# Optimization experiments

Measured on AMD Instinct MI355X. Metric: run time of the kernel, lower is better.

## Reference

```python
import jax, jax.numpy as jnp
import numpy as np

DIM = 1024
N_HEADS = 16
HEAD_DIM = DIM // N_HEADS


def setup_inputs() -> dict:
    key = jax.random.key(0)
    ks = jax.random.split(key, 6)
    s = DIM ** -0.5
    return {
        "x": jax.random.normal(ks[0], (2, 2048, DIM), dtype=jnp.float32),
        "Wq": jax.random.normal(ks[1], (DIM, DIM), dtype=jnp.float32) * s,
        "Wk": jax.random.normal(ks[2], (DIM, DIM), dtype=jnp.float32) * s,
        "Wv": jax.random.normal(ks[3], (DIM, DIM), dtype=jnp.float32) * s,
        "Wo": jax.random.normal(ks[4], (DIM, DIM), dtype=jnp.float32) * s,
        "bo": jax.random.normal(ks[5], (DIM,), dtype=jnp.float32) * 0.01,
    }


def reference(x, Wq, Wk, Wv, Wo, bo):
    B, T, C = x.shape
    H, D = N_HEADS, HEAD_DIM
    # Linear(dim, dim, bias=False): y = x @ W^T
    q = (x @ Wq.T).reshape(B, T, H, D).transpose(0, 2, 1, 3)  # B H T D
    k = (x @ Wk.T).reshape(B, T, H, D).transpose(0, 2, 1, 3)
    v = (x @ Wv.T).reshape(B, T, H, D).transpose(0, 2, 1, 3)
    q = q * (D ** -0.5)
    attn = jnp.einsum('bhqd,bhkd->bhqk', q, k)  # B H T T
    causal_mask = jnp.triu(jnp.ones((T, T), dtype=bool), k=1)
    attn = jnp.where(causal_mask, -jnp.inf, attn)
    attn = jax.nn.softmax(attn, axis=-1)
    out = jnp.einsum('bhqk,bhkd->bhqd', attn, v)  # B H T D
    out = out.transpose(0, 2, 1, 3).reshape(B, T, C)
    return out @ Wo.T + bo
```

## Files before the change

kernel.cpp:

```cpp
#include <hip/hip_runtime.h>
#include <math.h>

typedef __attribute__((ext_vector_type(8))) short bf16x8;
typedef __attribute__((ext_vector_type(4))) float f32x4;

__device__ __forceinline__ ushort f2bf(float f) {
  union { float f; unsigned u; } v; v.f = f;
  return (ushort)((v.u + 0x8000u) >> 16);
}

__device__ __forceinline__ void g2l16(const void* g, void* l) {
  __builtin_amdgcn_global_load_lds((const __attribute__((address_space(1))) unsigned*)g,
                                   (__attribute__((address_space(3))) unsigned*)l, 16, 0, 0);
}

__global__ __launch_bounds__(256) void cast_x_kernel(const float* __restrict__ x,
                                                     ushort* __restrict__ o, int n4) {
  int i = blockIdx.x * 256 + threadIdx.x;
  if (i >= n4) return;
  float4 v = ((const float4*)x)[i];
  ushort4 u; u.x = f2bf(v.x); u.y = f2bf(v.y); u.z = f2bf(v.z); u.w = f2bf(v.w);
  ((ushort4*)o)[i] = u;
}

__global__ __launch_bounds__(256) void cast_w_kernel(const float* __restrict__ Wq,
                                                     const float* __restrict__ Wk,
                                                     const float* __restrict__ Wv,
                                                     const float* __restrict__ Wo,
                                                     ushort* __restrict__ o) {
  int i = blockIdx.x * 256 + threadIdx.x;
  int row = i >> 8;
  int sel = row >> 10;
  const float* src = (sel == 0) ? Wq : (sel == 1) ? Wk : (sel == 2) ? Wv : Wo;
  float scale = (sel == 0) ? 0.125f * 1.44269504088896f : 1.0f;
  float4 v = ((const float4*)src)[i & 0x3FFFF];
  ushort4 u;
  u.x = f2bf(v.x * scale); u.y = f2bf(v.y * scale);
  u.z = f2bf(v.z * scale); u.w = f2bf(v.w * scale);
  ((ushort4*)o)[i] = u;
}

template<int BN, bool BF16_OUT, bool BIAS, bool SPLIT>
__global__ __launch_bounds__(256) void gemm_bt(const ushort* __restrict__ A,
                                               const ushort* __restrict__ B,
                                               void* __restrict__ Cout,
                                               const float* __restrict__ bias,
                                               int M, int N, int K) {
  __shared__ __align__(16) ushort As[2][128 * 32];
  __shared__ __align__(16) ushort Bs[2][BN * 32];
  const int m0 = blockIdx.y * 128, n0 = blockIdx.x * BN;
  const int tid = threadIdx.x, lane = tid & 63, wid = tid >> 6;
  const int quad = lane >> 4, lc = lane & 15;
  const int lrow = lane >> 2, lcol = (lane & 3) * 8;
  const int wm = (BN == 128) ? (wid >> 1) * 64 : wid * 32;
  const int wn = (BN == 128) ? (wid & 1) * 64 : 0;
  constexpr int MT = (BN == 128) ? 4 : 2;

  f32x4 acc[MT][4] = {};

  auto stage = [&](int k0, int nb) {
    const ushort* Ag = A + (size_t)(m0 + wid * 32 + lrow) * K + k0 + lcol;
    g2l16(Ag, &As[nb][wid * 1024]);
    g2l16(Ag + (size_t)16 * K, &As[nb][wid * 1024 + 512]);
    if constexpr (BN == 128) {
      const ushort* Bg = B + (size_t)(n0 + wid * 32 + lrow) * K + k0 + lcol;
      g2l16(Bg, &Bs[nb][wid * 1024]);
      g2l16(Bg + (size_t)16 * K, &Bs[nb][wid * 1024 + 512]);
    } else {
      const ushort* Bg = B + (size_t)(n0 + wid * 16 + lrow) * K + k0 + lcol;
      g2l16(Bg, &Bs[nb][wid * 512]);
    }
  };

  stage(0, 0);
  for (int k0 = 0; k0 < K; k0 += 32) {
    const int nb = (k0 >> 5) & 1;
    __syncthreads();
    if (k0 + 32 < K) stage(k0 + 32, nb ^ 1);

    bf16x8 af[MT], bfr[4];
#pragma unroll
    for (int t = 0; t < MT; t++)
      af[t] = *(const bf16x8*)&As[nb][(wm + t * 16 + lc) * 32 + quad * 8];
#pragma unroll
    for (int t = 0; t < 4; t++)
      bfr[t] = *(const bf16x8*)&Bs[nb][(wn + t * 16 + lc) * 32 + quad * 8];
#pragma unroll
    for (int mt = 0; mt < MT; mt++)
#pragma unroll
      for (int nt = 0; nt < 4; nt++)
        acc[mt][nt] = __builtin_amdgcn_mfma_f32_16x16x32_bf16(af[mt], bfr[nt], acc[mt][nt], 0, 0, 0);
  }

#pragma unroll
  for (int mt = 0; mt < MT; mt++) {
#pragma unroll
    for (int r = 0; r < 4; r++) {
      int row = m0 + wm + mt * 16 + quad * 4 + r;
#pragma unroll
      for (int nt = 0; nt < 4; nt++) {
        int col = n0 + wn + nt * 16 + lc;
        float v = acc[mt][nt][r];
        if (BIAS) v += bias[col];
        size_t dst;
        if (SPLIT) dst = ((size_t)(col >> 10) << 22) + (size_t)row * 1024 + (col & 1023);
        else       dst = (size_t)row * N + col;
        if (BF16_OUT) ((ushort*)Cout)[dst] = f2bf(v);
        else          ((float*)Cout)[dst]  = v;
      }
    }
  }
}

__global__ __launch_bounds__(256) void transpose_v(const ushort* __restrict__ Vb,
                                                   ushort* __restrict__ Vt) {
  __shared__ ushort tile[64][72];
  const int bh = blockIdx.y, b = bh >> 4, h = bh & 15;
  const int tt = blockIdx.x;
  const int tid = threadIdx.x;
#pragma unroll
  for (int i = 0; i < 2; i++) {
    int idx = i * 256 + tid;
    int trow = idx >> 3;
    int dcol = (idx & 7) * 8;
    uint4 v = *(const uint4*)(Vb + (size_t)(b * 2048 + tt * 64 + trow) * 1024 + h * 64 + dcol);
    ushort e[8]; *(uint4*)e = v;
#pragma unroll
    for (int j = 0; j < 8; j++) tile[dcol + j][trow] = e[j];
  }
  __syncthreads();
#pragma unroll
  for (int i = 0; i < 2; i++) {
    int idx = i * 256 + tid;
    int drow = idx >> 3;
    int tloc = (idx & 7) * 8;
    uint4 v = *(const uint4*)&tile[drow][tloc];
    *(uint4*)(Vt + (size_t)bh * 131072 + (size_t)drow * 2048 + tt * 64 + tloc) = v;
  }
}

__global__ __launch_bounds__(256, 2) void attn_kernel(const ushort* __restrict__ Qb,
                                                      const ushort* __restrict__ Kb,
                                                      const ushort* __restrict__ Vt,
                                                      ushort* __restrict__ Out) {
  __shared__ __align__(16) ushort Ks[2][2][64 * 32];
  __shared__ __align__(16) ushort Vs[2][2][64 * 32];
  __shared__ __align__(16) ushort Ps[4][32][72];

  const int bh = blockIdx.y, b = bh >> 4, h = bh & 15;
  const int bx = blockIdx.x;
  const int ord = (bx & 1) ? (bx >> 1) : (15 - (bx >> 1));
  const int qb_block = ord * 128;
  const int tid = threadIdx.x, lane = tid & 63, wid = tid >> 6;
  const int quad = lane >> 4, lc = lane & 15;
  const int lrow = lane >> 2, lcol = (lane & 3) * 8;
  const int qbw = qb_block + wid * 32;

  const size_t kbase = (size_t)(b * 2048) * 1024 + h * 64;
  const size_t vbase = (size_t)bh * 131072;

  bf16x8 qf[2][2];
#pragma unroll
  for (int t = 0; t < 2; t++) {
    const ushort* Qp = Qb + kbase + (size_t)(qbw + t * 16 + lc) * 1024;
    qf[t][0] = *(const bf16x8*)(Qp + quad * 8);
    qf[t][1] = *(const bf16x8*)(Qp + 32 + quad * 8);
  }

  f32x4 o_acc[2][4] = {};
  float l_r[2][4] = {};

  auto stage = [&](int kb, int nb) {
    const ushort* gK = Kb + kbase + (size_t)(kb + wid * 16 + lrow) * 1024 + lcol;
    g2l16(gK,      &Ks[nb][0][wid * 512]);
    g2l16(gK + 32, &Ks[nb][1][wid * 512]);
    const ushort* gV = Vt + vbase + (size_t)(wid * 16 + lrow) * 2048 + kb + lcol;
    g2l16(gV,      &Vs[nb][0][wid * 512]);
    g2l16(gV + 32, &Vs[nb][1][wid * 512]);
  };

  const int ntiles = (qb_block >> 6) + 2;
  stage(0, 0);
  for (int kt = 0; kt < ntiles; kt++) {
    const int kb = kt * 64;
    const int buf = kt & 1;
    __syncthreads();
    if (kt + 1 < ntiles) stage(kb + 64, buf ^ 1);

#pragma unroll
    for (int c = 0; c < 4; c++) {
      bf16x8 kf0 = *(const bf16x8*)&Ks[buf][0][(c * 16 + lc) * 32 + quad * 8];
      bf16x8 kf1 = *(const bf16x8*)&Ks[buf][1][(c * 16 + lc) * 32 + quad * 8];
#pragma unroll
      for (int t = 0; t < 2; t++) {
        f32x4 z = {};
        z = __builtin_amdgcn_mfma_f32_16x16x32_bf16(qf[t][0], kf0, z, 0, 0, 0);
        z = __builtin_amdgcn_mfma_f32_16x16x32_bf16(qf[t][1], kf1, z, 0, 0, 0);
        const bool diag = (kb + 63 > qbw + t * 16);
#pragma unroll
        for (int r = 0; r < 4; r++) {
          float sv = z[r];
          if (diag && (kb + c * 16 + lc > qbw + t * 16 + quad * 4 + r)) sv = -1e30f;
          float pv = exp2f(sv);
          l_r[t][r] += pv;
          Ps[wid][t * 16 + quad * 4 + r][c * 16 + lc] = f2bf(pv);
        }
      }
    }
    __asm__ volatile("s_waitcnt lgkmcnt(0)" ::: "memory");

    bf16x8 ap[2][2];
#pragma unroll
    for (int t = 0; t < 2; t++) {
      ap[t][0] = *(const bf16x8*)&Ps[wid][t * 16 + lc][quad * 8];
      ap[t][1] = *(const bf16x8*)&Ps[wid][t * 16 + lc][32 + quad * 8];
    }
#pragma unroll
    for (int nt = 0; nt < 4; nt++) {
      bf16x8 vb0 = *(const bf16x8*)&Vs[buf][0][(nt * 16 + lc) * 32 + quad * 8];
      bf16x8 vb1 = *(const bf16x8*)&Vs[buf][1][(nt * 16 + lc) * 32 + quad * 8];
#pragma unroll
      for (int t = 0; t < 2; t++) {
        o_acc[t][nt] = __builtin_amdgcn_mfma_f32_16x16x32_bf16(ap[t][0], vb0, o_acc[t][nt], 0, 0, 0);
        o_acc[t][nt] = __builtin_amdgcn_mfma_f32_16x16x32_bf16(ap[t][1], vb1, o_acc[t][nt], 0, 0, 0);
      }
    }
  }

#pragma unroll
  for (int t = 0; t < 2; t++)
#pragma unroll
    for (int r = 0; r < 4; r++) {
      float s_ = l_r[t][r];
      s_ += __shfl_xor(s_, 1);
      s_ += __shfl_xor(s_, 2);
      s_ += __shfl_xor(s_, 4);
      s_ += __shfl_xor(s_, 8);
      l_r[t][r] = 1.0f / s_;
    }
#pragma unroll
  for (int t = 0; t < 2; t++)
#pragma unroll
    for (int r = 0; r < 4; r++) {
      size_t orow = ((size_t)(b * 2048) + qbw + t * 16 + quad * 4 + r) * 1024 + h * 64 + lc;
#pragma unroll
      for (int nt = 0; nt < 4; nt++)
        Out[orow + nt * 16] = f2bf(o_acc[t][nt][r] * l_r[t][r]);
    }
}

extern "C" void kernel_launch(void* const* d_in, const int* in_sizes, int n_in,
                              void* d_out, int out_size, void* d_ws, size_t ws_size,
                              hipStream_t stream) {
  const float* x  = (const float*)d_in[0];
  const float* Wq = (const float*)d_in[1];
  const float* Wk = (const float*)d_in[2];
  const float* Wv = (const float*)d_in[3];
  const float* Wo = (const float*)d_in[4];
  const float* bo = (const float*)d_in[5];
  float* out = (float*)d_out;

  char* ws = (char*)d_ws;
  ushort* xbf  = (ushort*)(ws);
  ushort* wcat = (ushort*)(ws + (8ull  << 20));
  ushort* qkv  = (ushort*)(ws + (16ull << 20));
  ushort* Vt   = (ushort*)(ws);
  ushort* Qp   = qkv;
  ushort* Kp   = qkv + (1ull << 22);
  ushort* Vp   = qkv + (2ull << 22);
  ushort* attn_out = Vp;

  cast_x_kernel<<<4096, 256, 0, stream>>>(x, xbf, 1048576);
  cast_w_kernel<<<4096, 256, 0, stream>>>(Wq, Wk, Wv, Wo, wcat);

  gemm_bt<128, true, false, true><<<dim3(24, 32), 256, 0, stream>>>(
      xbf, wcat, qkv, nullptr, 4096, 3072, 1024);

  transpose_v<<<dim3(32, 32), 256, 0, stream>>>(Vp, Vt);

  attn_kernel<<<dim3(16, 32), 256, 0, stream>>>(Qp, Kp, Vt, attn_out);

  gemm_bt<64, false, true, false><<<dim3(16, 32), 256, 0, stream>>>(
      attn_out, wcat + (size_t)3072 * 1024, out, bo, 4096, 1024, 1024);
}
```

Baseline: 229.1 us.

## Split attention over key chunks with atomic fp32 accumulation and separate normalize

```diff
diff --git a/kernel.cpp b/kernel.cpp
--- a/kernel.cpp
+++ b/kernel.cpp
@@ -14,30 +14,29 @@
                                    (__attribute__((address_space(3))) unsigned*)l, 16, 0, 0);
 }
 
-__global__ __launch_bounds__(256) void cast_x_kernel(const float* __restrict__ x,
-                                                     ushort* __restrict__ o, int n4) {
+__global__ __launch_bounds__(256) void cast_all(const float* __restrict__ x,
+                                                const float* __restrict__ Wq,
+                                                const float* __restrict__ Wk,
+                                                const float* __restrict__ Wv,
+                                                const float* __restrict__ Wo,
+                                                ushort* __restrict__ xbf,
+                                                ushort* __restrict__ wcat) {
   int i = blockIdx.x * 256 + threadIdx.x;
-  if (i >= n4) return;
-  float4 v = ((const float4*)x)[i];
-  ushort4 u; u.x = f2bf(v.x); u.y = f2bf(v.y); u.z = f2bf(v.z); u.w = f2bf(v.w);
-  ((ushort4*)o)[i] = u;
-}
-
-__global__ __launch_bounds__(256) void cast_w_kernel(const float* __restrict__ Wq,
-                                                     const float* __restrict__ Wk,
-                                                     const float* __restrict__ Wv,
-                                                     const float* __restrict__ Wo,
-                                                     ushort* __restrict__ o) {
-  int i = blockIdx.x * 256 + threadIdx.x;
-  int row = i >> 8;
-  int sel = row >> 10;
-  const float* src = (sel == 0) ? Wq : (sel == 1) ? Wk : (sel == 2) ? Wv : Wo;
-  float scale = (sel == 0) ? 0.125f * 1.44269504088896f : 1.0f;
-  float4 v = ((const float4*)src)[i & 0x3FFFF];
-  ushort4 u;
-  u.x = f2bf(v.x * scale); u.y = f2bf(v.y * scale);
-  u.z = f2bf(v.z * scale); u.w = f2bf(v.w * scale);
-  ((ushort4*)o)[i] = u;
+  if (i < 1048576) {
+    float4 v = ((const float4*)x)[i];
+    ushort4 u; u.x = f2bf(v.x); u.y = f2bf(v.y); u.z = f2bf(v.z); u.w = f2bf(v.w);
+    ((ushort4*)xbf)[i] = u;
+  } else {
+    int j = i - 1048576;
+    int sel = j >> 18;
+    const float* src = (sel == 0) ? Wq : (sel == 1) ? Wk : (sel == 2) ? Wv : Wo;
+    float scale = (sel == 0) ? 0.125f * 1.44269504088896f : 1.0f;
+    float4 v = ((const float4*)src)[j & 0x3FFFF];
+    ushort4 u;
+    u.x = f2bf(v.x * scale); u.y = f2bf(v.y * scale);
+    u.z = f2bf(v.z * scale); u.w = f2bf(v.w * scale);
+    ((ushort4*)wcat)[j] = u;
+  }
 }
 
 template<int BN, bool BF16_OUT, bool BIAS, bool SPLIT>
@@ -139,114 +138,122 @@
   }
 }
 
-__global__ __launch_bounds__(256, 2) void attn_kernel(const ushort* __restrict__ Qb,
+__global__ __launch_bounds__(256, 6) void attn_kernel(const ushort* __restrict__ Qb,
                                                       const ushort* __restrict__ Kb,
                                                       const ushort* __restrict__ Vt,
-                                                      ushort* __restrict__ Out) {
-  __shared__ __align__(16) ushort Ks[2][2][64 * 32];
-  __shared__ __align__(16) ushort Vs[2][2][64 * 32];
-  __shared__ __align__(16) ushort Ps[4][32][72];
+                                                      float* __restrict__ O32,
+                                                      float* __restrict__ L32) {
+  __shared__ __align__(16) ushort Ks[2][64 * 32];
+  __shared__ __align__(16) ushort Vs[2][64 * 32];
+  __shared__ __align__(16) ushort Ps[4][16][72];
 
   const int bh = blockIdx.y, b = bh >> 4, h = bh & 15;
-  const int bx = blockIdx.x;
-  const int ord = (bx & 1) ? (bx >> 1) : (15 - (bx >> 1));
-  const int qb_block = ord * 128;
+  const int f = 79 - (int)blockIdx.x;
+  int qi, ci;
+  if (f < 8)       { qi = f;                 ci = 0; }
+  else if (f < 24) { int g = f - 8;  qi = 8  + (g >> 1); ci = g & 1; }
+  else if (f < 48) { int g = f - 24; int q3 = g / 3; qi = 16 + q3; ci = g - 3 * q3; }
+  else             { int g = f - 48; qi = 24 + (g >> 2); ci = g & 3; }
+
+  const int t0 = ci * 8;
+  const int t1 = min(t0 + 8, qi + 1);
+  const int qb_block = qi * 64;
+
   const int tid = threadIdx.x, lane = tid & 63, wid = tid >> 6;
   const int quad = lane >> 4, lc = lane & 15;
   const int lrow = lane >> 2, lcol = (lane & 3) * 8;
-  const int qbw = qb_block + wid * 32;
+  const int qbw = qb_block + wid * 16;
 
   const size_t kbase = (size_t)(b * 2048) * 1024 + h * 64;
   const size_t vbase = (size_t)bh * 131072;
 
-  bf16x8 qf[2][2];
-#pragma unroll
-  for (int t = 0; t < 2; t++) {
-    const ushort* Qp = Qb + kbase + (size_t)(qbw + t * 16 + lc) * 1024;
-    qf[t][0] = *(const bf16x8*)(Qp + quad * 8);
-    qf[t][1] = *(const bf16x8*)(Qp + 32 + quad * 8);
-  }
-
-  f32x4 o_acc[2][4] = {};
-  float l_r[2][4] = {};
-
-  auto stage = [&](int kb, int nb) {
-    const ushort* gK = Kb + kbase + (size_t)(kb + wid * 16 + lrow) * 1024 + lcol;
-    g2l16(gK,      &Ks[nb][0][wid * 512]);
-    g2l16(gK + 32, &Ks[nb][1][wid * 512]);
-    const ushort* gV = Vt + vbase + (size_t)(wid * 16 + lrow) * 2048 + kb + lcol;
-    g2l16(gV,      &Vs[nb][0][wid * 512]);
-    g2l16(gV + 32, &Vs[nb][1][wid * 512]);
-  };
-
-  const int ntiles = (qb_block >> 6) + 2;
-  stage(0, 0);
-  for (int kt = 0; kt < ntiles; kt++) {
+  const ushort* Qp = Qb + kbase + (size_t)(qbw + lc) * 1024;
+  bf16x8 qf0 = *(const bf16x8*)(Qp + quad * 8);
+  bf16x8 qf1 = *(const bf16x8*)(Qp + 32 + quad * 8);
+
+  f32x4 o_acc[4] = {};
+  float l_r[4] = {0.f, 0.f, 0.f, 0.f};
+
+  for (int kt = t0; kt < t1; kt++) {
     const int kb = kt * 64;
-    const int buf = kt & 1;
     __syncthreads();
-    if (kt + 1 < ntiles) stage(kb + 64, buf ^ 1);
-
+#pragma unroll
+    for (int cc = 0; cc < 2; cc++) {
+      int ck = wid + cc * 4;
+      int half = ck >> 2, rg = ck & 3;
+      const ushort* gK = Kb + kbase + (size_t)(kb + rg * 16 + lrow) * 1024 + half * 32 + lcol;
+      g2l16(gK, &Ks[half][rg * 512]);
+      const ushort* gV = Vt + vbase + (size_t)(rg * 16 + lrow) * 2048 + kb + half * 32 + lcol;
+      g2l16(gV, &Vs[half][rg * 512]);
+    }
+    __syncthreads();
+
+    const bool diag = (kb + 63 > qbw);
 #pragma unroll
     for (int c = 0; c < 4; c++) {
-      bf16x8 kf0 = *(const bf16x8*)&Ks[buf][0][(c * 16 + lc) * 32 + quad * 8];
-      bf16x8 kf1 = *(const bf16x8*)&Ks[buf][1][(c * 16 + lc) * 32 + quad * 8];
-#pragma unroll
-      for (int t = 0; t < 2; t++) {
-        f32x4 z = {};
-        z = __builtin_amdgcn_mfma_f32_16x16x32_bf16(qf[t][0], kf0, z, 0, 0, 0);
-        z = __builtin_amdgcn_mfma_f32_16x16x32_bf16(qf[t][1], kf1, z, 0, 0, 0);
-        const bool diag = (kb + 63 > qbw + t * 16);
-#pragma unroll
-        for (int r = 0; r < 4; r++) {
-          float sv = z[r];
-          if (diag && (kb + c * 16 + lc > qbw + t * 16 + quad * 4 + r)) sv = -1e30f;
-          float pv = exp2f(sv);
-          l_r[t][r] += pv;
-          Ps[wid][t * 16 + quad * 4 + r][c * 16 + lc] = f2bf(pv);
-        }
+      bf16x8 kf0 = *(const bf16x8*)&Ks[0][(c * 16 + lc) * 32 + quad * 8];
+      bf16x8 kf1 = *(const bf16x8*)&Ks[1][(c * 16 + lc) * 32 + quad * 8];
+      f32x4 z = {};
+      z = __builtin_amdgcn_mfma_f32_16x16x32_bf16(qf0, kf0, z, 0, 0, 0);
+      z = __builtin_amdgcn_mfma_f32_16x16x32_bf16(qf1, kf1, z, 0, 0, 0);
+#pragma unroll
+      for (int r = 0; r < 4; r++) {
+        float sv = z[r];
+        if (diag && (kb + c * 16 + lc > qbw + quad * 4 + r)) sv = -1e30f;
+        float pv = __builtin_amdgcn_exp2f(sv);
+        l_r[r] += pv;
+        Ps[wid][quad * 4 + r][c * 16 + lc] = f2bf(pv);
       }
     }
     __asm__ volatile("s_waitcnt lgkmcnt(0)" ::: "memory");
-
-    bf16x8 ap[2][2];
-#pragma unroll
-    for (int t = 0; t < 2; t++) {
-      ap[t][0] = *(const bf16x8*)&Ps[wid][t * 16 + lc][quad * 8];
-      ap[t][1] = *(const bf16x8*)&Ps[wid][t * 16 + lc][32 + quad * 8];
-    }
+    bf16x8 ap0 = *(const bf16x8*)&Ps[wid][lc][quad * 8];
+    bf16x8 ap1 = *(const bf16x8*)&Ps[wid][lc][32 + quad * 8];
+
 #pragma unroll
     for (int nt = 0; nt < 4; nt++) {
-      bf16x8 vb0 = *(const bf16x8*)&Vs[buf][0][(nt * 16 + lc) * 32 + quad * 8];
-      bf16x8 vb1 = *(const bf16x8*)&Vs[buf][1][(nt * 16 + lc) * 32 + quad * 8];
-#pragma unroll
-      for (int t = 0; t < 2; t++) {
-        o_acc[t][nt] = __builtin_amdgcn_mfma_f32_16x16x32_bf16(ap[t][0], vb0, o_acc[t][nt], 0, 0, 0);
-        o_acc[t][nt] = __builtin_amdgcn_mfma_f32_16x16x32_bf16(ap[t][1], vb1, o_acc[t][nt], 0, 0, 0);
-      }
-    }
-  }
-
-#pragma unroll
-  for (int t = 0; t < 2; t++)
-#pragma unroll
-    for (int r = 0; r < 4; r++) {
-      float s_ = l_r[t][r];
-      s_ += __shfl_xor(s_, 1);
-      s_ += __shfl_xor(s_, 2);
-      s_ += __shfl_xor(s_, 4);
-      s_ += __shfl_xor(s_, 8);
-      l_r[t][r] = 1.0f / s_;
-    }
-#pragma unroll
-  for (int t = 0; t < 2; t++)
-#pragma unroll
-    for (int r = 0; r < 4; r++) {
-      size_t orow = ((size_t)(b * 2048) + qbw + t * 16 + quad * 4 + r) * 1024 + h * 64 + lc;
-#pragma unroll
-      for (int nt = 0; nt < 4; nt++)
-        Out[orow + nt * 16] = f2bf(o_acc[t][nt][r] * l_r[t][r]);
-    }
+      bf16x8 vb0 = *(const bf16x8*)&Vs[0][(nt * 16 + lc) * 32 + quad * 8];
+      bf16x8 vb1 = *(const bf16x8*)&Vs[1][(nt * 16 + lc) * 32 + quad * 8];
+      o_acc[nt] = __builtin_amdgcn_mfma_f32_16x16x32_bf16(ap0, vb0, o_acc[nt], 0, 0, 0);
+      o_acc[nt] = __builtin_amdgcn_mfma_f32_16x16x32_bf16(ap1, vb1, o_acc[nt], 0, 0, 0);
+    }
+  }
+
+#pragma unroll
+  for (int r = 0; r < 4; r++) {
+    float s_ = l_r[r];
+    s_ += __shfl_xor(s_, 1);
+    s_ += __shfl_xor(s_, 2);
+    s_ += __shfl_xor(s_, 4);
+    s_ += __shfl_xor(s_, 8);
+    l_r[r] = s_;
+  }
+  if (lc == 0) {
+#pragma unroll
+    for (int r = 0; r < 4; r++)
+      atomicAdd(&L32[(size_t)bh * 2048 + qbw + quad * 4 + r], l_r[r]);
+  }
+#pragma unroll
+  for (int r = 0; r < 4; r++) {
+    size_t orow = ((size_t)(b * 2048) + qbw + quad * 4 + r) * 1024 + h * 64 + lc;
+#pragma unroll
+    for (int nt = 0; nt < 4; nt++)
+      atomicAdd(&O32[orow + nt * 16], o_acc[nt][r]);
+  }
+}
+
+__global__ __launch_bounds__(256) void normalize_kernel(const float* __restrict__ O32,
+                                                        const float* __restrict__ L32,
+                                                        ushort* __restrict__ Out) {
+  const int row = blockIdx.x;
+  const int tid = threadIdx.x;
+  const int col = tid * 4;
+  const int b = row >> 11, t = row & 2047, h = col >> 6;
+  const float inv = 1.0f / L32[(size_t)(b * 16 + h) * 2048 + t];
+  float4 o = ((const float4*)(O32 + (size_t)row * 1024))[tid];
+  ushort4 u;
+  u.x = f2bf(o.x * inv); u.y = f2bf(o.y * inv);
+  u.z = f2bf(o.z * inv); u.w = f2bf(o.w * inv);
+  ((ushort4*)(Out + (size_t)row * 1024))[tid] = u;
 }
 
 extern "C" void kernel_launch(void* const* d_in, const int* in_sizes, int n_in,
@@ -268,17 +275,23 @@
   ushort* Qp   = qkv;
   ushort* Kp   = qkv + (1ull << 22);
   ushort* Vp   = qkv + (2ull << 22);
-  ushort* attn_out = Vp;
-
-  cast_x_kernel<<<4096, 256, 0, stream>>>(x, xbf, 1048576);
-  cast_w_kernel<<<4096, 256, 0, stream>>>(Wq, Wk, Wv, Wo, wcat);
+  float*  L32  = (float*)Vp;
+  float*  O32  = out;
+  ushort* attn_out = Qp;
+
+  cast_all<<<8192, 256, 0, stream>>>(x, Wq, Wk, Wv, Wo, xbf, wcat);
 
   gemm_bt<128, true, false, true><<<dim3(24, 32), 256, 0, stream>>>(
       xbf, wcat, qkv, nullptr, 4096, 3072, 1024);
 
   transpose_v<<<dim3(32, 32), 256, 0, stream>>>(Vp, Vt);
 
-  attn_kernel<<<dim3(16, 32), 256, 0, stream>>>(Qp, Kp, Vt, attn_out);
+  hipMemsetAsync(O32, 0, (size_t)4096 * 1024 * 4, stream);
+  hipMemsetAsync(L32, 0, (size_t)32 * 2048 * 4, stream);
+
+  attn_kernel<<<dim3(80, 32), 256, 0, stream>>>(Qp, Kp, Vt, O32, L32);
+
+  normalize_kernel<<<4096, 256, 0, stream>>>(O32, L32, attn_out);
 
   gemm_bt<64, false, true, false><<<dim3(16, 32), 256, 0, stream>>>(
       attn_out, wcat + (size_t)3072 * 1024, out, bo, 4096, 1024, 1024);
```

Result: faster. 212.4 us (-7.3%).
